# Optimization experiments

Hardware: AMD Instinct MI355X
Metric: run time of the kernel (lower is better)

The kernel has to match this reference:

```python
import jax, jax.numpy as jnp
import numpy as np

HEADS = 4
DIM_HEAD = 32
SCALE = DIM_HEAD ** -0.5
EPS = 1e-5


def setup_inputs() -> dict:
    key = jax.random.key(0)
    ks = jax.random.split(key, 5)
    b, c, h, w = 32, 256, 64, 64
    hidden = HEADS * DIM_HEAD  # 128
    return {
        "x": jax.random.normal(ks[0], (b, c, h, w), dtype=jnp.float32),
        "Wqkv": jax.random.normal(ks[1], (3 * hidden, c), dtype=jnp.float32) * 0.05,
        "bqkv": jax.random.normal(ks[2], (3 * hidden,), dtype=jnp.float32) * 0.05,
        "Wout": jax.random.normal(ks[3], (c, hidden), dtype=jnp.float32) * 0.05,
        "bout": jax.random.normal(ks[4], (c,), dtype=jnp.float32) * 0.05,
        "gamma": jnp.ones((c,), dtype=jnp.float32),
        "beta": jnp.zeros((c,), dtype=jnp.float32),
    }


def reference(x, Wqkv, bqkv, Wout, bout, gamma, beta):
    b, c, h, w = x.shape
    n = h * w
    # 1x1 conv == per-pixel linear: [b,c,h,w] x [3*hidden,c] -> [b,3*hidden,h,w]
    qkv = jnp.einsum('bchw,oc->bohw', x, Wqkv) + bqkv[None, :, None, None]
    q, k, v = jnp.split(qkv, 3, axis=1)
    # b (heads dh) x y -> b heads dh n
    q = q.reshape(b, HEADS, DIM_HEAD, n)
    k = k.reshape(b, HEADS, DIM_HEAD, n)
    v = v.reshape(b, HEADS, DIM_HEAD, n)
    q = jax.nn.softmax(q, axis=-2) * SCALE  # softmax over dim_head axis
    k = jax.nn.softmax(k, axis=-2)
    context = jnp.einsum('bhdn,bhen->bhde', k, v)   # [b,h,dh,dh]
    out = jnp.einsum('bhde,bhdn->bhen', context, q)  # [b,h,dh,n]
    out = out.reshape(b, HEADS * DIM_HEAD, h, w)
    # 1x1 conv projection back to dim
    out = jnp.einsum('bchw,oc->bohw', out, Wout) + bout[None, :, None, None]
    # GroupNorm(1, dim): normalize over (C,H,W) per sample, affine per channel
    mu = jnp.mean(out, axis=(1, 2, 3), keepdims=True)
    var = jnp.var(out, axis=(1, 2, 3), keepdims=True)
    out = (out - mu) * jax.lax.rsqrt(var + EPS)
    return out * gamma[None, :, None, None] + beta[None, :, None, None]
```

## Files before the change

### kernel.cpp

```cpp
#include <hip/hip_runtime.h>
#include <math.h>


#define NPIX 4096
#define SCALE 0.17677669529663687f

typedef __bf16 bf16;
typedef __bf16 bf16x4 __attribute__((ext_vector_type(4)));
typedef __bf16 bf16x8 __attribute__((ext_vector_type(8)));
typedef float  f32x4  __attribute__((ext_vector_type(4)));

__global__ __launch_bounds__(256) void k0_convert(
    const float* __restrict__ Wqkv, const float* __restrict__ Wout,
    bf16* __restrict__ wqkv_bf, bf16* __restrict__ wout_bf)
{
    int i = blockIdx.x * 256 + threadIdx.x;
    if (i < 98304) wqkv_bf[i] = (bf16)Wqkv[i];
    else           wout_bf[i - 98304] = (bf16)Wout[i - 98304];
}

__global__ __launch_bounds__(256, 4) void k1_qkv(
    const float* __restrict__ x, const bf16* __restrict__ wqkv_bf,
    const float* __restrict__ bqkv, bf16* __restrict__ q_wsT,
    bf16* __restrict__ part)
{
    __shared__ __align__(16) bf16 sm[18432];
    bf16* xT = sm;

    const int blk  = blockIdx.x;
    const int b    = blk >> 6;
    const int n0   = (blk & 63) << 6;
    const int tid  = threadIdx.x;
    const int lane = tid & 63;
    const int s    = __builtin_amdgcn_readfirstlane(tid >> 6);
    const int m16  = lane & 15;
    const int quad = lane >> 4;

    const float* xb = x + (size_t)b * (256 * NPIX) + n0;
    {
        const int px  = tid & 63;
        const int cq0 = tid >> 6;
        float vv[16][4];
        #pragma unroll
        for (int it = 0; it < 16; ++it) {
            const float* xp = xb + (size_t)(cq0 + 4*it) * 4 * NPIX + px;
            vv[it][0] = xp[0];
            vv[it][1] = xp[NPIX];
            vv[it][2] = xp[2*NPIX];
            vv[it][3] = xp[3*NPIX];
        }
        #pragma unroll
        for (int it = 0; it < 16; ++it) {
            int cq = cq0 + 4*it;
            int g  = cq >> 1;
            int o  = (cq & 1) * 4;
            int gp = g ^ (px & 7);
            bf16x4 pk = { (bf16)vv[it][0], (bf16)vv[it][1],
                          (bf16)vv[it][2], (bf16)vv[it][3] };
            *(bf16x4*)&xT[px*256 + gp*8 + o] = pk;
        }
    }
    __syncthreads();

    {
        f32x4 qacc[2][4] = {};
        for (int kc = 0; kc < 8; ++kc) {
            bf16x8 bfr[4];
            #pragma unroll
            for (int nt = 0; nt < 4; ++nt) {
                int px = nt*16 + m16;
                int gp = (kc*4 + quad) ^ (px & 7);
                bfr[nt] = *(const bf16x8*)&xT[px*256 + gp*8];
            }
            #pragma unroll
            for (int mt = 0; mt < 2; ++mt) {
                int row = s*32 + mt*16 + m16;
                bf16x8 afr = *(const bf16x8*)&wqkv_bf[(size_t)row*256 + kc*32 + quad*8];
                #pragma unroll
                for (int nt = 0; nt < 4; ++nt)
                    qacc[mt][nt] = __builtin_amdgcn_mfma_f32_16x16x32_bf16(afr, bfr[nt], qacc[mt][nt], 0, 0, 0);
            }
        }
        float bq[8];
        #pragma unroll
        for (int j = 0; j < 8; ++j)
            bq[j] = bqkv[s*32 + (j >> 2)*16 + quad*4 + (j & 3)];

        #pragma unroll
        for (int nt = 0; nt < 4; ++nt) {
            float v[8]; float mx = -1e30f;
            #pragma unroll
            for (int j = 0; j < 8; ++j) { v[j] = qacc[j>>2][nt][j&3] + bq[j]; mx = fmaxf(mx, v[j]); }
            mx = fmaxf(mx, __shfl_xor(mx, 16));
            mx = fmaxf(mx, __shfl_xor(mx, 32));
            float sum = 0.f;
            #pragma unroll
            for (int j = 0; j < 8; ++j) { v[j] = __expf(v[j] - mx); sum += v[j]; }
            sum += __shfl_xor(sum, 16);
            sum += __shfl_xor(sum, 32);
            float rs = SCALE / sum;
            size_t rowb = (size_t)(b*4096 + n0 + nt*16 + m16) * 128;
            #pragma unroll
            for (int mt = 0; mt < 2; ++mt) {
                bf16x4 pk = { (bf16)(v[mt*4+0]*rs), (bf16)(v[mt*4+1]*rs),
                              (bf16)(v[mt*4+2]*rs), (bf16)(v[mt*4+3]*rs) };
                *(bf16x4*)&q_wsT[rowb + s*32 + mt*16 + quad*4] = pk;
            }
        }
    }

    f32x4 acc[4][4] = {};
    for (int kc = 0; kc < 8; ++kc) {
        bf16x8 bfr[4];
        #pragma unroll
        for (int nt = 0; nt < 4; ++nt) {
            int px = nt*16 + m16;
            int gp = (kc*4 + quad) ^ (px & 7);
            bfr[nt] = *(const bf16x8*)&xT[px*256 + gp*8];
        }
        #pragma unroll
        for (int mt = 0; mt < 4; ++mt) {
            int row = 128 + (mt >> 1)*128 + s*32 + (mt & 1)*16 + m16;
            bf16x8 afr = *(const bf16x8*)&wqkv_bf[(size_t)row*256 + kc*32 + quad*8];
            #pragma unroll
            for (int nt = 0; nt < 4; ++nt)
                acc[mt][nt] = __builtin_amdgcn_mfma_f32_16x16x32_bf16(afr, bfr[nt], acc[mt][nt], 0, 0, 0);
        }
    }

    float bk[8], bv[8];
    #pragma unroll
    for (int j = 0; j < 8; ++j) {
        int rr = (j >> 2)*16 + quad*4 + (j & 3);
        bk[j] = bqkv[128 + s*32 + rr];
        bv[j] = bqkv[256 + s*32 + rr];
    }

    __syncthreads();
    bf16* kl = sm + s*2304;
    bf16* vl = sm + 9216 + s*2304;
    #pragma unroll
    for (int nt = 0; nt < 4; ++nt) {
        float v[8]; float mx = -1e30f;
        #pragma unroll
        for (int j = 0; j < 8; ++j) { v[j] = acc[j>>2][nt][j&3] + bk[j]; mx = fmaxf(mx, v[j]); }
        mx = fmaxf(mx, __shfl_xor(mx, 16));
        mx = fmaxf(mx, __shfl_xor(mx, 32));
        float sum = 0.f;
        #pragma unroll
        for (int j = 0; j < 8; ++j) { v[j] = __expf(v[j] - mx); sum += v[j]; }
        sum += __shfl_xor(sum, 16);
        sum += __shfl_xor(sum, 32);
        float rs = 1.f / sum;
        #pragma unroll
        for (int j = 0; j < 8; ++j) {
            int d  = (j>>2)*16 + quad*4 + (j&3);
            int px = nt*16 + m16;
            kl[d*72 + px] = (bf16)(v[j] * rs);
            vl[d*72 + px] = (bf16)(acc[2 + (j>>2)][nt][j&3] + bv[j]);
        }
    }
    __syncthreads();

    f32x4 cacc[2][2] = {};
    #pragma unroll
    for (int ks = 0; ks < 2; ++ks) {
        bf16x8 ak[2], bvv[2];
        #pragma unroll
        for (int mt = 0; mt < 2; ++mt)
            ak[mt] = *(const bf16x8*)&kl[(mt*16 + m16)*72 + ks*32 + quad*8];
        #pragma unroll
        for (int nt = 0; nt < 2; ++nt)
            bvv[nt] = *(const bf16x8*)&vl[(nt*16 + m16)*72 + ks*32 + quad*8];
        #pragma unroll
        for (int mt = 0; mt < 2; ++mt)
            #pragma unroll
            for (int nt = 0; nt < 2; ++nt)
                cacc[mt][nt] = __builtin_amdgcn_mfma_f32_16x16x32_bf16(ak[mt], bvv[nt], cacc[mt][nt], 0, 0, 0);
    }
    bf16* pdst = part + (size_t)blk * 4096 + s*1024;
    #pragma unroll
    for (int mt = 0; mt < 2; ++mt)
        #pragma unroll
        for (int nt = 0; nt < 2; ++nt)
            #pragma unroll
            for (int r = 0; r < 4; ++r)
                pdst[(mt*16 + quad*4 + r)*32 + nt*16 + m16] = (bf16)cacc[mt][nt][r];
}

__global__ __launch_bounds__(256) void k2_reduce(
    const bf16* __restrict__ part, bf16* __restrict__ ctxT_bf)
{
    int i = blockIdx.x * 256 + threadIdx.x;
    int b = i >> 12, r = i & 4095;
    const bf16* p = part + (size_t)b * 64 * 4096 + r;
    float sum = 0.f;
    #pragma unroll 8
    for (int j = 0; j < 64; ++j) sum += (float)p[(size_t)j * 4096];
    int h = r >> 10, d = (r >> 5) & 31, e = r & 31;
    ctxT_bf[(size_t)((b*4 + h)*32 + e)*32 + d] = (bf16)sum;
}

__global__ __launch_bounds__(256) void k3_out(
    const bf16* __restrict__ q_wsT, const bf16* __restrict__ ctxT_bf,
    const bf16* __restrict__ wout_bf, const float* __restrict__ bout,
    float* __restrict__ out, float* __restrict__ gstats)
{
    __shared__ __align__(16) bf16 attnT[8192];
    __shared__ float red[512];
    const int blk  = blockIdx.x;
    const int b    = blk >> 6;
    const int n0   = (blk & 63) << 6;
    const int tid  = threadIdx.x;
    const int lane = tid & 63;
    const int s    = __builtin_amdgcn_readfirstlane(tid >> 6);
    const int m16  = lane & 15;
    const int quad = lane >> 4;

    f32x4 aacc[2][4] = {};
    {
        bf16x8 afr[2], bfr[4];
        const bf16* ctxs = ctxT_bf + (size_t)(b*4 + s) * 1024;
        #pragma unroll
        for (int mt = 0; mt < 2; ++mt)
            afr[mt] = *(const bf16x8*)&ctxs[(mt*16 + m16)*32 + quad*8];
        const bf16* qb = q_wsT + (size_t)(b*4096 + n0) * 128 + s*32;
        #pragma unroll
        for (int nt = 0; nt < 4; ++nt)
            bfr[nt] = *(const bf16x8*)&qb[(size_t)(nt*16 + m16)*128 + quad*8];
        #pragma unroll
        for (int mt = 0; mt < 2; ++mt)
            #pragma unroll
            for (int nt = 0; nt < 4; ++nt)
                aacc[mt][nt] = __builtin_amdgcn_mfma_f32_16x16x32_bf16(afr[mt], bfr[nt], aacc[mt][nt], 0, 0, 0);
    }

    #pragma unroll
    for (int mt = 0; mt < 2; ++mt)
        #pragma unroll
        for (int nt = 0; nt < 4; ++nt) {
            int p   = nt*16 + m16;
            int chb = s*32 + mt*16 + quad*4;
            int gp  = (chb >> 3) ^ m16;
            bf16x4 pk = { (bf16)aacc[mt][nt][0], (bf16)aacc[mt][nt][1],
                          (bf16)aacc[mt][nt][2], (bf16)aacc[mt][nt][3] };
            *(bf16x4*)&attnT[p*128 + gp*8 + (quad & 1)*4] = pk;
        }
    __syncthreads();

    f32x4 acc[4][4] = {};
    const bf16* wb = wout_bf + (size_t)s * 64 * 128;
    for (int kc = 0; kc < 4; ++kc) {
        bf16x8 wfr[4], xfr[4];
        #pragma unroll
        for (int mt = 0; mt < 4; ++mt)
            wfr[mt] = *(const bf16x8*)&wb[(size_t)(mt*16 + m16)*128 + kc*32 + quad*8];
        #pragma unroll
        for (int nt = 0; nt < 4; ++nt) {
            int p  = nt*16 + m16;
            int gp = (kc*4 + quad) ^ m16;
            xfr[nt] = *(const bf16x8*)&attnT[p*128 + gp*8];
        }
        #pragma unroll
        for (int mt = 0; mt < 4; ++mt)
            #pragma unroll
            for (int nt = 0; nt < 4; ++nt)
                acc[mt][nt] = __builtin_amdgcn_mfma_f32_16x16x32_bf16(wfr[mt], xfr[nt], acc[mt][nt], 0, 0, 0);
    }

    float ls = 0.f, lss = 0.f;
    float* ob = out + ((size_t)b*256 + s*64) * NPIX + n0;
    #pragma unroll
    for (int mt = 0; mt < 4; ++mt) {
        #pragma unroll
        for (int r = 0; r < 4; ++r) {
            int o = mt*16 + quad*4 + r;
            float bo = bout[s*64 + o];
            #pragma unroll
            for (int nt = 0; nt < 4; ++nt) {
                float v = acc[mt][nt][r] + bo;
                ob[(size_t)o*NPIX + nt*16 + m16] = v;
                ls += v; lss += v*v;
            }
        }
    }

    red[tid] = ls; red[256 + tid] = lss;
    __syncthreads();
    for (int off = 128; off > 0; off >>= 1) {
        if (tid < off) {
            red[tid]       += red[tid + off];
            red[256 + tid] += red[256 + tid + off];
        }
        __syncthreads();
    }
    if (tid == 0) {
        atomicAdd(&gstats[b],      red[0]);
        atomicAdd(&gstats[32 + b], red[256]);
    }
}

__global__ void k4_stats(float* __restrict__ gstats)
{
    int t = threadIdx.x;
    if (t < 32) {
        const float inv_cnt = 1.0f / 1048576.0f;
        float m   = gstats[t] * inv_cnt;
        float var = gstats[32 + t] * inv_cnt - m*m;
        gstats[64 + t] = m;
        gstats[96 + t] = rsqrtf(var + 1e-5f);
    }
}

__global__ __launch_bounds__(256) void k5_norm(
    float* __restrict__ out, const float* __restrict__ gstats,
    const float* __restrict__ gamma, const float* __restrict__ beta)
{
    size_t gid  = (size_t)blockIdx.x * 256 + threadIdx.x;
    size_t base = gid * 4;
    int b = (int)(base >> 20);
    int o = (int)((base >> 12) & 255);
    float m   = gstats[64 + b];
    float inv = gstats[96 + b];
    float a = inv * gamma[o];
    float c = beta[o] - m * a;
    float4 v = ((float4*)out)[gid];
    v.x = v.x * a + c; v.y = v.y * a + c;
    v.z = v.z * a + c; v.w = v.w * a + c;
    ((float4*)out)[gid] = v;
}

extern "C" void kernel_launch(void* const* d_in, const int* in_sizes, int n_in,
                              void* d_out, int out_size, void* d_ws, size_t ws_size,
                              hipStream_t stream) {
    const float* x     = (const float*)d_in[0];
    const float* Wqkv  = (const float*)d_in[1];
    const float* bqkv  = (const float*)d_in[2];
    const float* Wout  = (const float*)d_in[3];
    const float* bout  = (const float*)d_in[4];
    const float* gamma = (const float*)d_in[5];
    const float* beta  = (const float*)d_in[6];
    float* out = (float*)d_out;
    float* ws  = (float*)d_ws;

    bf16*  q_wsT   = (bf16*)ws;
    bf16*  wqkv_bf = (bf16*)(ws + 8388608);
    bf16*  wout_bf = (bf16*)(ws + 8437760);
    bf16*  ctxT_bf = (bf16*)(ws + 8454144);
    bf16*  part    = (bf16*)(ws + 16777216);
    float* gstats  = ws + 25165824;

    hipMemsetAsync(gstats, 0, 64 * sizeof(float), stream);
    k0_convert<<<512,  256, 0, stream>>>(Wqkv, Wout, wqkv_bf, wout_bf);
    k1_qkv    <<<2048, 256, 0, stream>>>(x, wqkv_bf, bqkv, q_wsT, part);
    k2_reduce <<<512,  256, 0, stream>>>(part, ctxT_bf);
    k3_out    <<<2048, 256, 0, stream>>>(q_wsT, ctxT_bf, wout_bf, bout, out, gstats);
    k4_stats  <<<1,     64, 0, stream>>>(gstats);
    k5_norm   <<<32768,256, 0, stream>>>(out, gstats, gamma, beta);
}
```

Before: 368.9 us.

## Make k1 persistent with next-tile x prefetch; split k3 output GEMM into halves

k1_qkv now launches half as many blocks, and each block loops over two tiles. It prefetches the next tile's x slice into registers during the K/V softmax and context phase, then writes it into LDS after the current tile finishes, so global load latency overlaps compute. k3_out computes its 64 output channels in two halves of 32, which shrinks the accumulator footprint, and adds an occupancy hint of 4 waves. The prefetch adds register pressure and extra barriers in k1, and the grid halving may leave fewer blocks in flight to hide latency.

```diff
diff --git a/kernel.cpp b/kernel.cpp
--- a/kernel.cpp
+++ b/kernel.cpp
@@ -4,6 +4,7 @@
 
 #define NPIX 4096
 #define SCALE 0.17677669529663687f
+#define K1_GRID 1024
 
 typedef __bf16 bf16;
 typedef __bf16 bf16x4 __attribute__((ext_vector_type(4)));
@@ -27,19 +28,17 @@
     __shared__ __align__(16) bf16 sm[18432];
     bf16* xT = sm;
 
-    const int blk  = blockIdx.x;
-    const int b    = blk >> 6;
-    const int n0   = (blk & 63) << 6;
     const int tid  = threadIdx.x;
     const int lane = tid & 63;
     const int s    = __builtin_amdgcn_readfirstlane(tid >> 6);
     const int m16  = lane & 15;
     const int quad = lane >> 4;
-
-    const float* xb = x + (size_t)b * (256 * NPIX) + n0;
+    const int px   = tid & 63;
+    const int cq0  = tid >> 6;
+
     {
-        const int px  = tid & 63;
-        const int cq0 = tid >> 6;
+        const int t0 = blockIdx.x;
+        const float* xb = x + (size_t)(t0 >> 6) * (256 * NPIX) + ((t0 & 63) << 6);
         float vv[16][4];
         #pragma unroll
         for (int it = 0; it < 16; ++it) {
@@ -49,48 +48,121 @@
             vv[it][2] = xp[2*NPIX];
             vv[it][3] = xp[3*NPIX];
         }
+        __builtin_amdgcn_sched_barrier(0);
         #pragma unroll
         for (int it = 0; it < 16; ++it) {
             int cq = cq0 + 4*it;
-            int g  = cq >> 1;
-            int o  = (cq & 1) * 4;
-            int gp = g ^ (px & 7);
+            int gp = (cq >> 1) ^ (px & 7);
             bf16x4 pk = { (bf16)vv[it][0], (bf16)vv[it][1],
                           (bf16)vv[it][2], (bf16)vv[it][3] };
-            *(bf16x4*)&xT[px*256 + gp*8 + o] = pk;
+            *(bf16x4*)&xT[px*256 + gp*8 + (cq & 1)*4] = pk;
         }
     }
     __syncthreads();
 
-    {
-        f32x4 qacc[2][4] = {};
+    #pragma unroll 1
+    for (int t = blockIdx.x; t < 2048; t += K1_GRID) {
+        const int b   = t >> 6;
+        const int n0  = (t & 63) << 6;
+        const int tn  = t + K1_GRID;
+        const bool pf = tn < 2048;
+        const float* xbn = x + (size_t)(tn >> 6) * (256 * NPIX) + ((tn & 63) << 6);
+
+        {
+            f32x4 qacc[2][4] = {};
+            for (int kc = 0; kc < 8; ++kc) {
+                bf16x8 bfr[4];
+                #pragma unroll
+                for (int nt = 0; nt < 4; ++nt) {
+                    int p  = nt*16 + m16;
+                    int gp = (kc*4 + quad) ^ (p & 7);
+                    bfr[nt] = *(const bf16x8*)&xT[p*256 + gp*8];
+                }
+                #pragma unroll
+                for (int mt = 0; mt < 2; ++mt) {
+                    int row = s*32 + mt*16 + m16;
+                    bf16x8 afr = *(const bf16x8*)&wqkv_bf[(size_t)row*256 + kc*32 + quad*8];
+                    #pragma unroll
+                    for (int nt = 0; nt < 4; ++nt)
+                        qacc[mt][nt] = __builtin_amdgcn_mfma_f32_16x16x32_bf16(afr, bfr[nt], qacc[mt][nt], 0, 0, 0);
+                }
+            }
+            float bq[8];
+            #pragma unroll
+            for (int j = 0; j < 8; ++j)
+                bq[j] = bqkv[s*32 + (j >> 2)*16 + quad*4 + (j & 3)];
+
+            #pragma unroll
+            for (int nt = 0; nt < 4; ++nt) {
+                float v[8]; float mx = -1e30f;
+                #pragma unroll
+                for (int j = 0; j < 8; ++j) { v[j] = qacc[j>>2][nt][j&3] + bq[j]; mx = fmaxf(mx, v[j]); }
+                mx = fmaxf(mx, __shfl_xor(mx, 16));
+                mx = fmaxf(mx, __shfl_xor(mx, 32));
+                float sum = 0.f;
+                #pragma unroll
+                for (int j = 0; j < 8; ++j) { v[j] = __expf(v[j] - mx); sum += v[j]; }
+                sum += __shfl_xor(sum, 16);
+                sum += __shfl_xor(sum, 32);
+                float rs = SCALE / sum;
+                size_t rowb = (size_t)(b*4096 + n0 + nt*16 + m16) * 128;
+                #pragma unroll
+                for (int mt = 0; mt < 2; ++mt) {
+                    bf16x4 pk = { (bf16)(v[mt*4+0]*rs), (bf16)(v[mt*4+1]*rs),
+                                  (bf16)(v[mt*4+2]*rs), (bf16)(v[mt*4+3]*rs) };
+                    *(bf16x4*)&q_wsT[rowb + s*32 + mt*16 + quad*4] = pk;
+                }
+            }
+        }
+
+        f32x4 acc[4][4] = {};
         for (int kc = 0; kc < 8; ++kc) {
             bf16x8 bfr[4];
             #pragma unroll
             for (int nt = 0; nt < 4; ++nt) {
-                int px = nt*16 + m16;
-                int gp = (kc*4 + quad) ^ (px & 7);
-                bfr[nt] = *(const bf16x8*)&xT[px*256 + gp*8];
-            }
-            #pragma unroll
-            for (int mt = 0; mt < 2; ++mt) {
-                int row = s*32 + mt*16 + m16;
+                int p  = nt*16 + m16;
+                int gp = (kc*4 + quad) ^ (p & 7);
+                bfr[nt] = *(const bf16x8*)&xT[p*256 + gp*8];
+            }
+            #pragma unroll
+            for (int mt = 0; mt < 4; ++mt) {
+                int row = 128 + (mt >> 1)*128 + s*32 + (mt & 1)*16 + m16;
                 bf16x8 afr = *(const bf16x8*)&wqkv_bf[(size_t)row*256 + kc*32 + quad*8];
                 #pragma unroll
                 for (int nt = 0; nt < 4; ++nt)
-                    qacc[mt][nt] = __builtin_amdgcn_mfma_f32_16x16x32_bf16(afr, bfr[nt], qacc[mt][nt], 0, 0, 0);
-            }
-        }
-        float bq[8];
-        #pragma unroll
-        for (int j = 0; j < 8; ++j)
-            bq[j] = bqkv[s*32 + (j >> 2)*16 + quad*4 + (j & 3)];
-
+                    acc[mt][nt] = __builtin_amdgcn_mfma_f32_16x16x32_bf16(afr, bfr[nt], acc[mt][nt], 0, 0, 0);
+            }
+        }
+
+        float bk[8], bv[8];
+        #pragma unroll
+        for (int j = 0; j < 8; ++j) {
+            int rr = (j >> 2)*16 + quad*4 + (j & 3);
+            bk[j] = bqkv[128 + s*32 + rr];
+            bv[j] = bqkv[256 + s*32 + rr];
+        }
+
+        float pv[8][4];
+        if (pf) {
+            #pragma unroll
+            for (int it = 0; it < 8; ++it) {
+                const float* xp = xbn + (size_t)(cq0 + 4*it) * 4 * NPIX + px;
+                pv[it][0] = xp[0];
+                pv[it][1] = xp[NPIX];
+                pv[it][2] = xp[2*NPIX];
+                pv[it][3] = xp[3*NPIX];
+            }
+            __builtin_amdgcn_sched_barrier(0);
+        }
+
+        __syncthreads();
+        bf16* kl = sm + s*2304;
+        bf16* vl = sm + 9216 + s*2304;
         #pragma unroll
         for (int nt = 0; nt < 4; ++nt) {
             float v[8]; float mx = -1e30f;
             #pragma unroll
-            for (int j = 0; j < 8; ++j) { v[j] = qacc[j>>2][nt][j&3] + bq[j]; mx = fmaxf(mx, v[j]); }
+            for (int j = 0; j < 8; ++j) { v[j] = acc[j>>2][nt][j&3] + bk[j]; mx = fmaxf(mx, v[j]); }
             mx = fmaxf(mx, __shfl_xor(mx, 16));
             mx = fmaxf(mx, __shfl_xor(mx, 32));
             float sum = 0.f;
@@ -98,94 +170,73 @@
             for (int j = 0; j < 8; ++j) { v[j] = __expf(v[j] - mx); sum += v[j]; }
             sum += __shfl_xor(sum, 16);
             sum += __shfl_xor(sum, 32);
-            float rs = SCALE / sum;
-            size_t rowb = (size_t)(b*4096 + n0 + nt*16 + m16) * 128;
-            #pragma unroll
-            for (int mt = 0; mt < 2; ++mt) {
-                bf16x4 pk = { (bf16)(v[mt*4+0]*rs), (bf16)(v[mt*4+1]*rs),
-                              (bf16)(v[mt*4+2]*rs), (bf16)(v[mt*4+3]*rs) };
-                *(bf16x4*)&q_wsT[rowb + s*32 + mt*16 + quad*4] = pk;
-            }
-        }
-    }
-
-    f32x4 acc[4][4] = {};
-    for (int kc = 0; kc < 8; ++kc) {
-        bf16x8 bfr[4];
-        #pragma unroll
-        for (int nt = 0; nt < 4; ++nt) {
-            int px = nt*16 + m16;
-            int gp = (kc*4 + quad) ^ (px & 7);
-            bfr[nt] = *(const bf16x8*)&xT[px*256 + gp*8];
-        }
-        #pragma unroll
-        for (int mt = 0; mt < 4; ++mt) {
-            int row = 128 + (mt >> 1)*128 + s*32 + (mt & 1)*16 + m16;
-            bf16x8 afr = *(const bf16x8*)&wqkv_bf[(size_t)row*256 + kc*32 + quad*8];
-            #pragma unroll
-            for (int nt = 0; nt < 4; ++nt)
-                acc[mt][nt] = __builtin_amdgcn_mfma_f32_16x16x32_bf16(afr, bfr[nt], acc[mt][nt], 0, 0, 0);
-        }
-    }
-
-    float bk[8], bv[8];
-    #pragma unroll
-    for (int j = 0; j < 8; ++j) {
-        int rr = (j >> 2)*16 + quad*4 + (j & 3);
-        bk[j] = bqkv[128 + s*32 + rr];
-        bv[j] = bqkv[256 + s*32 + rr];
-    }
-
-    __syncthreads();
-    bf16* kl = sm + s*2304;
-    bf16* vl = sm + 9216 + s*2304;
-    #pragma unroll
-    for (int nt = 0; nt < 4; ++nt) {
-        float v[8]; float mx = -1e30f;
-        #pragma unroll
-        for (int j = 0; j < 8; ++j) { v[j] = acc[j>>2][nt][j&3] + bk[j]; mx = fmaxf(mx, v[j]); }
-        mx = fmaxf(mx, __shfl_xor(mx, 16));
-        mx = fmaxf(mx, __shfl_xor(mx, 32));
-        float sum = 0.f;
-        #pragma unroll
-        for (int j = 0; j < 8; ++j) { v[j] = __expf(v[j] - mx); sum += v[j]; }
-        sum += __shfl_xor(sum, 16);
-        sum += __shfl_xor(sum, 32);
-        float rs = 1.f / sum;
-        #pragma unroll
-        for (int j = 0; j < 8; ++j) {
-            int d  = (j>>2)*16 + quad*4 + (j&3);
-            int px = nt*16 + m16;
-            kl[d*72 + px] = (bf16)(v[j] * rs);
-            vl[d*72 + px] = (bf16)(acc[2 + (j>>2)][nt][j&3] + bv[j]);
-        }
-    }
-    __syncthreads();
-
-    f32x4 cacc[2][2] = {};
-    #pragma unroll
-    for (int ks = 0; ks < 2; ++ks) {
-        bf16x8 ak[2], bvv[2];
+            float rs = 1.f / sum;
+            #pragma unroll
+            for (int j = 0; j < 8; ++j) {
+                int d = (j>>2)*16 + quad*4 + (j&3);
+                int p = nt*16 + m16;
+                kl[d*72 + p] = (bf16)(v[j] * rs);
+                vl[d*72 + p] = (bf16)(acc[2 + (j>>2)][nt][j&3] + bv[j]);
+            }
+        }
+        __syncthreads();
+
+        f32x4 cacc[2][2] = {};
+        #pragma unroll
+        for (int ks = 0; ks < 2; ++ks) {
+            bf16x8 ak[2], bvv[2];
+            #pragma unroll
+            for (int mt = 0; mt < 2; ++mt)
+                ak[mt] = *(const bf16x8*)&kl[(mt*16 + m16)*72 + ks*32 + quad*8];
+            #pragma unroll
+            for (int nt = 0; nt < 2; ++nt)
+                bvv[nt] = *(const bf16x8*)&vl[(nt*16 + m16)*72 + ks*32 + quad*8];
+            #pragma unroll
+            for (int mt = 0; mt < 2; ++mt)
+                #pragma unroll
+                for (int nt = 0; nt < 2; ++nt)
+                    cacc[mt][nt] = __builtin_amdgcn_mfma_f32_16x16x32_bf16(ak[mt], bvv[nt], cacc[mt][nt], 0, 0, 0);
+        }
+        bf16* pdst = part + (size_t)t * 4096 + s*1024;
         #pragma unroll
         for (int mt = 0; mt < 2; ++mt)
-            ak[mt] = *(const bf16x8*)&kl[(mt*16 + m16)*72 + ks*32 + quad*8];
-        #pragma unroll
-        for (int nt = 0; nt < 2; ++nt)
-            bvv[nt] = *(const bf16x8*)&vl[(nt*16 + m16)*72 + ks*32 + quad*8];
-        #pragma unroll
-        for (int mt = 0; mt < 2; ++mt)
             #pragma unroll
             for (int nt = 0; nt < 2; ++nt)
-                cacc[mt][nt] = __builtin_amdgcn_mfma_f32_16x16x32_bf16(ak[mt], bvv[nt], cacc[mt][nt], 0, 0, 0);
-    }
-    bf16* pdst = part + (size_t)blk * 4096 + s*1024;
-    #pragma unroll
-    for (int mt = 0; mt < 2; ++mt)
-        #pragma unroll
-        for (int nt = 0; nt < 2; ++nt)
-            #pragma unroll
-            for (int r = 0; r < 4; ++r)
-                pdst[(mt*16 + quad*4 + r)*32 + nt*16 + m16] = (bf16)cacc[mt][nt][r];
+                #pragma unroll
+                for (int r = 0; r < 4; ++r)
+                    pdst[(mt*16 + quad*4 + r)*32 + nt*16 + m16] = (bf16)cacc[mt][nt][r];
+
+        if (pf) {
+            __syncthreads();
+            #pragma unroll
+            for (int it = 0; it < 8; ++it) {
+                int cq = cq0 + 4*it;
+                int gp = (cq >> 1) ^ (px & 7);
+                bf16x4 pk = { (bf16)pv[it][0], (bf16)pv[it][1],
+                              (bf16)pv[it][2], (bf16)pv[it][3] };
+                *(bf16x4*)&xT[px*256 + gp*8 + (cq & 1)*4] = pk;
+            }
+            float qv[8][4];
+            #pragma unroll
+            for (int it = 0; it < 8; ++it) {
+                const float* xp = xbn + (size_t)(cq0 + 4*(it + 8)) * 4 * NPIX + px;
+                qv[it][0] = xp[0];
+                qv[it][1] = xp[NPIX];
+                qv[it][2] = xp[2*NPIX];
+                qv[it][3] = xp[3*NPIX];
+            }
+            __builtin_amdgcn_sched_barrier(0);
+            #pragma unroll
+            for (int it = 0; it < 8; ++it) {
+                int cq = cq0 + 4*(it + 8);
+                int gp = (cq >> 1) ^ (px & 7);
+                bf16x4 pk = { (bf16)qv[it][0], (bf16)qv[it][1],
+                              (bf16)qv[it][2], (bf16)qv[it][3] };
+                *(bf16x4*)&xT[px*256 + gp*8 + (cq & 1)*4] = pk;
+            }
+            __syncthreads();
+        }
+    }
 }
 
 __global__ __launch_bounds__(256) void k2_reduce(
@@ -201,7 +252,7 @@
     ctxT_bf[(size_t)((b*4 + h)*32 + e)*32 + d] = (bf16)sum;
 }
 
-__global__ __launch_bounds__(256) void k3_out(
+__global__ __launch_bounds__(256, 4) void k3_out(
     const bf16* __restrict__ q_wsT, const bf16* __restrict__ ctxT_bf,
     const bf16* __restrict__ wout_bf, const float* __restrict__ bout,
     float* __restrict__ out, float* __restrict__ gstats)
@@ -248,39 +299,42 @@
         }
     __syncthreads();
 
-    f32x4 acc[4][4] = {};
-    const bf16* wb = wout_bf + (size_t)s * 64 * 128;
-    for (int kc = 0; kc < 4; ++kc) {
-        bf16x8 wfr[4], xfr[4];
-        #pragma unroll
-        for (int mt = 0; mt < 4; ++mt)
-            wfr[mt] = *(const bf16x8*)&wb[(size_t)(mt*16 + m16)*128 + kc*32 + quad*8];
-        #pragma unroll
-        for (int nt = 0; nt < 4; ++nt) {
-            int p  = nt*16 + m16;
-            int gp = (kc*4 + quad) ^ m16;
-            xfr[nt] = *(const bf16x8*)&attnT[p*128 + gp*8];
-        }
-        #pragma unroll
-        for (int mt = 0; mt < 4; ++mt)
-            #pragma unroll
-            for (int nt = 0; nt < 4; ++nt)
-                acc[mt][nt] = __builtin_amdgcn_mfma_f32_16x16x32_bf16(wfr[mt], xfr[nt], acc[mt][nt], 0, 0, 0);
-    }
-
     float ls = 0.f, lss = 0.f;
     float* ob = out + ((size_t)b*256 + s*64) * NPIX + n0;
-    #pragma unroll
-    for (int mt = 0; mt < 4; ++mt) {
-        #pragma unroll
-        for (int r = 0; r < 4; ++r) {
-            int o = mt*16 + quad*4 + r;
-            float bo = bout[s*64 + o];
+    #pragma unroll 1
+    for (int h = 0; h < 2; ++h) {
+        f32x4 acc[2][4] = {};
+        const bf16* wb = wout_bf + (size_t)(s*64 + h*32) * 128;
+        for (int kc = 0; kc < 4; ++kc) {
+            bf16x8 wfr[2], xfr[4];
+            #pragma unroll
+            for (int mt = 0; mt < 2; ++mt)
+                wfr[mt] = *(const bf16x8*)&wb[(size_t)(mt*16 + m16)*128 + kc*32 + quad*8];
             #pragma unroll
             for (int nt = 0; nt < 4; ++nt) {
-                float v = acc[mt][nt][r] + bo;
-                ob[(size_t)o*NPIX + nt*16 + m16] = v;
-                ls += v; lss += v*v;
+                int p  = nt*16 + m16;
+                int gp = (kc*4 + quad) ^ m16;
+                xfr[nt] = *(const bf16x8*)&attnT[p*128 + gp*8];
+            }
+            #pragma unroll
+            for (int mt = 0; mt < 2; ++mt)
+                #pragma unroll
+                for (int nt = 0; nt < 4; ++nt)
+                    acc[mt][nt] = __builtin_amdgcn_mfma_f32_16x16x32_bf16(wfr[mt], xfr[nt], acc[mt][nt], 0, 0, 0);
+        }
+
+        #pragma unroll
+        for (int mt = 0; mt < 2; ++mt) {
+            #pragma unroll
+            for (int r = 0; r < 4; ++r) {
+                int o = h*32 + mt*16 + quad*4 + r;
+                float bo = bout[s*64 + o];
+                #pragma unroll
+                for (int nt = 0; nt < 4; ++nt) {
+                    float v = acc[mt][nt][r] + bo;
+                    ob[(size_t)o*NPIX + nt*16 + m16] = v;
+                    ls += v; lss += v*v;
+                }
             }
         }
     }
@@ -351,10 +405,10 @@
     float* gstats  = ws + 25165824;
 
     hipMemsetAsync(gstats, 0, 64 * sizeof(float), stream);
-    k0_convert<<<512,  256, 0, stream>>>(Wqkv, Wout, wqkv_bf, wout_bf);
-    k1_qkv    <<<2048, 256, 0, stream>>>(x, wqkv_bf, bqkv, q_wsT, part);
-    k2_reduce <<<512,  256, 0, stream>>>(part, ctxT_bf);
-    k3_out    <<<2048, 256, 0, stream>>>(q_wsT, ctxT_bf, wout_bf, bout, out, gstats);
-    k4_stats  <<<1,     64, 0, stream>>>(gstats);
-    k5_norm   <<<32768,256, 0, stream>>>(out, gstats, gamma, beta);
-}
+    k0_convert<<<512,     256, 0, stream>>>(Wqkv, Wout, wqkv_bf, wout_bf);
+    k1_qkv    <<<K1_GRID, 256, 0, stream>>>(x, wqkv_bf, bqkv, q_wsT, part);
+    k2_reduce <<<512,     256, 0, stream>>>(part, ctxT_bf);
+    k3_out    <<<2048,    256, 0, stream>>>(q_wsT, ctxT_bf, wout_bf, bout, out, gstats);
+    k4_stats  <<<1,        64, 0, stream>>>(gstats);
+    k5_norm   <<<32768,   256, 0, stream>>>(out, gstats, gamma, beta);
+}
```

After: 532.0 us. 1.44x slower.
